# Kernel optimization log

Hardware: AMD Instinct MI355X
Metric: run time of the kernel (lower is better)

The kernel has to match this reference:

```python
import jax, jax.numpy as jnp
import numpy as np

QMIN, QMAX = -128, 127


def setup_inputs() -> dict:
    key = jax.random.key(0)
    kx, kw, kb = jax.random.split(key, 3)
    B, S, IN, OUT = 4, 2048, 4096, 4096
    x = jax.random.normal(kx, (B, S, IN), dtype=jnp.float32)
    # int8-valued weight stored as int32 for portability
    weight_int = jax.random.randint(kw, (OUT, IN), QMIN, QMAX + 1, dtype=jnp.int32)
    bias = jax.random.normal(kb, (OUT,), dtype=jnp.float32) * 0.02
    # plausible frozen qparams: x~N(0,1) -> range ~[-4,4]; weight range ~[-3,3] pre-quant
    scale_a = jnp.asarray(8.0 / 255.0, dtype=jnp.float32)
    zp_a = jnp.asarray(0, dtype=jnp.int32)
    weight_scale = jnp.asarray(6.0 / 255.0, dtype=jnp.float32)
    weight_zero_point = jnp.asarray(0, dtype=jnp.int32)
    return {
        "x": x,
        "weight_int": weight_int,
        "bias": bias,
        "scale_a": scale_a,
        "zp_a": zp_a,
        "weight_scale": weight_scale,
        "weight_zero_point": weight_zero_point,
    }


def reference(x, weight_int, bias, scale_a, zp_a, weight_scale, weight_zero_point):
    # fake-quantize activations: round(x/scale)+zp, clamp to int8 range
    zp_a_f = zp_a.astype(jnp.float32)
    x_int8 = jnp.clip(jnp.round(x / scale_a) + zp_a_f, QMIN, QMAX)
    x_cent = x_int8 - zp_a_f                                   # [B,S,IN]
    w_cent = weight_int.astype(jnp.float32) - weight_zero_point.astype(jnp.float32)  # [OUT,IN]
    y = jnp.einsum("bsi,oi->bso", x_cent, w_cent)              # dequant-space GEMM
    y = y * (scale_a * weight_scale)
    y = y + bias
    return y
```

## Files before the change

### kernel.cpp

```cpp
#include <hip/hip_runtime.h>
#include <stdint.h>

typedef int v4i  __attribute__((ext_vector_type(4)));
typedef int v16i __attribute__((ext_vector_type(16)));

__global__ void quant_x_kernel(const float* __restrict__ x,
                               int8_t* __restrict__ xq,
                               int* __restrict__ sum_x,
                               const float* __restrict__ p_scale,
                               const int* __restrict__ p_zp,
                               int K) {
    const int row = blockIdx.x;
    const int t = threadIdx.x;
    const float s = p_scale[0];
    const float zpf = (float)p_zp[0];
    const float* xr = x + (size_t)row * K;
    int8_t* qr = xq + (size_t)row * K;
    int lsum = 0;
    const int nchunk = K >> 10;
    for (int i = 0; i < nchunk; ++i) {
        const int idx = (i << 10) + (t << 2);
        const float4 v = *reinterpret_cast<const float4*>(xr + idx);
        const float f0 = fminf(fmaxf(rintf(v.x / s) + zpf, -128.f), 127.f);
        const float f1 = fminf(fmaxf(rintf(v.y / s) + zpf, -128.f), 127.f);
        const float f2 = fminf(fmaxf(rintf(v.z / s) + zpf, -128.f), 127.f);
        const float f3 = fminf(fmaxf(rintf(v.w / s) + zpf, -128.f), 127.f);
        const int i0 = (int)f0, i1 = (int)f1, i2 = (int)f2, i3 = (int)f3;
        lsum += i0 + i1 + i2 + i3;
        const unsigned pk = (unsigned)(i0 & 255) | ((unsigned)(i1 & 255) << 8) |
                            ((unsigned)(i2 & 255) << 16) | ((unsigned)(i3 & 255) << 24);
        *reinterpret_cast<unsigned*>(qr + idx) = pk;
    }
    __shared__ int wsum[4];
    #pragma unroll
    for (int off = 32; off > 0; off >>= 1) lsum += __shfl_down(lsum, off);
    if ((t & 63) == 0) wsum[t >> 6] = lsum;
    __syncthreads();
    if (t == 0) sum_x[row] = wsum[0] + wsum[1] + wsum[2] + wsum[3];
}

__global__ void quant_w_kernel(const int* __restrict__ w,
                               int8_t* __restrict__ wq,
                               int* __restrict__ sum_w,
                               int K) {
    const int row = blockIdx.x;
    const int t = threadIdx.x;
    const int* wr_ = w + (size_t)row * K;
    int8_t* qr = wq + (size_t)row * K;
    int lsum = 0;
    const int nchunk = K >> 10;
    for (int i = 0; i < nchunk; ++i) {
        const int idx = (i << 10) + (t << 2);
        const int4 v = *reinterpret_cast<const int4*>(wr_ + idx);
        lsum += v.x + v.y + v.z + v.w;
        const unsigned pk = (unsigned)(v.x & 255) | ((unsigned)(v.y & 255) << 8) |
                            ((unsigned)(v.z & 255) << 16) | ((unsigned)(v.w & 255) << 24);
        *reinterpret_cast<unsigned*>(qr + idx) = pk;
    }
    __shared__ int wsum[4];
    #pragma unroll
    for (int off = 32; off > 0; off >>= 1) lsum += __shfl_down(lsum, off);
    if ((t & 63) == 0) wsum[t >> 6] = lsum;
    __syncthreads();
    if (t == 0) sum_w[row] = wsum[0] + wsum[1] + wsum[2] + wsum[3];
}

#define BM 256
#define BN 256
#define BKB 128

__device__ __forceinline__ void gload_lds16(const void* g, void* l) {
    __builtin_amdgcn_global_load_lds(
        (const __attribute__((address_space(1))) unsigned int*)g,
        (__attribute__((address_space(3))) unsigned int*)l, 16, 0, 0);
}

#define MFMA_I8 __builtin_amdgcn_mfma_i32_32x32x32_i8

__global__ __launch_bounds__(512, 1)
void gemm_i8_kernel(const int8_t* __restrict__ xq,
                    const int8_t* __restrict__ wq,
                    const int* __restrict__ sum_x,
                    const int* __restrict__ sum_w,
                    const float* __restrict__ bias,
                    float* __restrict__ out,
                    const float* __restrict__ p_sa,
                    const int* __restrict__ p_zpa,
                    const float* __restrict__ p_sw,
                    const int* __restrict__ p_wzp,
                    int M, int N, int K) {
    __shared__ v4i ldsA[2][4][512];
    __shared__ v4i ldsB[2][4][512];

    const int tid = threadIdx.x;
    const int lane = tid & 63;
    const int wid = tid >> 6;
    const int wr = wid >> 2;
    const int wc = wid & 3;

    const int nwgy = M / BM;
    const int nwg = nwgy * (N / BN);
    const int bid = blockIdx.x;
    const int v = (bid & 7) * (nwg >> 3) + (bid >> 3);
    const int m0 = (v % nwgy) * BM;
    const int n0 = (v / nwgy) * BN;

    const int srow = wid * 32 + (lane >> 1);
    const int sj = (lane & 1) ^ ((lane >> 5) & 1);
    const int8_t* aS = xq + (size_t)(m0 + srow) * K + sj * 16;
    const int8_t* bS = wq + (size_t)(n0 + srow) * K + sj * 16;
    const int dbase = wid * 64;

    const int jp = (lane >> 5) ^ ((lane >> 4) & 1);
    const int l31 = lane & 31;
    const int aU = (wr * 128 + l31) * 2 + jp;
    const int bU = (wc * 64 + l31) * 2 + jp;

    v16i acc[4][2] = {};
    const int NT = K / BKB;

#define SLICE_STAGE(TT, S) do {                                               \
        gload_lds16(aS + (size_t)(TT) * BKB + (S) * 32,                       \
                    &ldsA[(TT) & 1][S][dbase]);                               \
        gload_lds16(bS + (size_t)(TT) * BKB + (S) * 32,                       \
                    &ldsB[(TT) & 1][S][dbase]);                               \
    } while (0)

    SLICE_STAGE(0, 0); SLICE_STAGE(0, 1); SLICE_STAGE(0, 2); SLICE_STAGE(0, 3);
    SLICE_STAGE(1, 0); SLICE_STAGE(1, 1); SLICE_STAGE(1, 2);
    asm volatile("s_waitcnt vmcnt(6)" ::: "memory");
    __builtin_amdgcn_sched_barrier(0);
    __builtin_amdgcn_s_barrier();

#define PHASE(P) do {                                                         \
        const v4i* LA = ldsA[t & 1][P];                                       \
        const v4i* LB = ldsB[t & 1][P];                                       \
        const v4i a0 = LA[aU];                                                \
        const v4i a1 = LA[aU + 64];                                           \
        const v4i a2 = LA[aU + 128];                                          \
        const v4i a3 = LA[aU + 192];                                          \
        const v4i b0 = LB[bU];                                                \
        const v4i b1 = LB[bU + 64];                                           \
        if (P == 0) { if (t <= NT - 2) SLICE_STAGE(t + 1, 3); }               \
        else        { if (t <= NT - 3) SLICE_STAGE(t + 2, P - 1); }           \
        __builtin_amdgcn_s_barrier();                                         \
        __builtin_amdgcn_s_setprio(1);                                        \
        acc[0][0] = MFMA_I8(a0, b0, acc[0][0], 0, 0, 0);                      \
        acc[0][1] = MFMA_I8(a0, b1, acc[0][1], 0, 0, 0);                      \
        acc[1][0] = MFMA_I8(a1, b0, acc[1][0], 0, 0, 0);                      \
        acc[1][1] = MFMA_I8(a1, b1, acc[1][1], 0, 0, 0);                      \
        acc[2][0] = MFMA_I8(a2, b0, acc[2][0], 0, 0, 0);                      \
        acc[2][1] = MFMA_I8(a2, b1, acc[2][1], 0, 0, 0);                      \
        acc[3][0] = MFMA_I8(a3, b0, acc[3][0], 0, 0, 0);                      \
        acc[3][1] = MFMA_I8(a3, b1, acc[3][1], 0, 0, 0);                      \
        __builtin_amdgcn_s_setprio(0);                                        \
        if (t < NT - 1) { asm volatile("s_waitcnt vmcnt(6)" ::: "memory"); }  \
        else            { asm volatile("s_waitcnt vmcnt(0)" ::: "memory"); }  \
        __builtin_amdgcn_sched_barrier(0);                                    \
        __builtin_amdgcn_s_barrier();                                         \
    } while (0)

    for (int t = 0; t < NT; ++t) {
        PHASE(0); PHASE(1); PHASE(2); PHASE(3);
    }
#undef PHASE
#undef SLICE_STAGE

    const float stot = p_sa[0] * p_sw[0];
    const int zpa = p_zpa[0];
    const int wzp = p_wzp[0];
    const int kzz = K * zpa * wzp;
    const int coll = lane & 31;
    const int rhi = (lane >> 5) * 4;

    #pragma unroll
    for (int cf = 0; cf < 2; ++cf) {
        const int cg = n0 + wc * 64 + cf * 32 + coll;
        const int sw = sum_w[cg];
        const float bb = bias[cg];
        #pragma unroll
        for (int rf = 0; rf < 4; ++rf) {
            const int rbase = m0 + wr * 128 + rf * 32 + rhi;
            #pragma unroll
            for (int r = 0; r < 16; ++r) {
                const int rowg = rbase + (r & 3) + 8 * (r >> 2);
                const int iv = acc[rf][cf][r] - wzp * sum_x[rowg] - zpa * sw + kzz;
                out[(size_t)rowg * N + cg] = (float)iv * stot + bb;
            }
        }
    }
}

extern "C" void kernel_launch(void* const* d_in, const int* in_sizes, int n_in,
                              void* d_out, int out_size, void* d_ws, size_t ws_size,
                              hipStream_t stream) {
    const float* x     = (const float*)d_in[0];
    const int*   w     = (const int*)d_in[1];
    const float* bias  = (const float*)d_in[2];
    const float* p_sa  = (const float*)d_in[3];
    const int*   p_zpa = (const int*)d_in[4];
    const float* p_sw  = (const float*)d_in[5];
    const int*   p_wzp = (const int*)d_in[6];

    const int N = in_sizes[2];
    const int K = in_sizes[1] / N;
    const int M = in_sizes[0] / K;

    int8_t* xq = (int8_t*)d_ws;
    int8_t* wq = xq + (size_t)M * K;
    int* sum_x = (int*)(wq + (size_t)N * K);
    int* sum_w = sum_x + M;

    quant_x_kernel<<<M, 256, 0, stream>>>(x, xq, sum_x, p_sa, p_zpa, K);
    quant_w_kernel<<<N, 256, 0, stream>>>(w, wq, sum_w, K);

    const int nwg = (M / BM) * (N / BN);
    gemm_i8_kernel<<<nwg, 512, 0, stream>>>(xq, wq, sum_x, sum_w, bias,
                                            (float*)d_out, p_sa, p_zpa, p_sw, p_wzp,
                                            M, N, K);
}
```

Before: 263.2 us.

## Load A fragments directly to registers and stage only B through LDS

The int8 GEMM no longer stages the activation tile through shared memory. Each wave loads its A fragments straight from global memory into registers, double-buffered across K steps. Only the weight tile goes through LDS, now with K-step 64 and an XOR swizzle. This cuts LDS traffic and footprint and halves the per-iteration barrier count, at the cost of more global traffic for A (redundant across the four column waves) and a full vmcnt(0) wait every tile, which gives shallower prefetch.

```diff
diff --git a/kernel.cpp b/kernel.cpp
--- a/kernel.cpp
+++ b/kernel.cpp
@@ -67,7 +67,7 @@
 
 #define BM 256
 #define BN 256
-#define BKB 128
+#define BKB 64
 
 __device__ __forceinline__ void gload_lds16(const void* g, void* l) {
     __builtin_amdgcn_global_load_lds(
@@ -89,8 +89,7 @@
                     const float* __restrict__ p_sw,
                     const int* __restrict__ p_wzp,
                     int M, int N, int K) {
-    __shared__ v4i ldsA[2][4][512];
-    __shared__ v4i ldsB[2][4][512];
+    __shared__ v4i ldsB[2][1024];
 
     const int tid = threadIdx.x;
     const int lane = tid & 63;
@@ -105,66 +104,83 @@
     const int m0 = (v % nwgy) * BM;
     const int n0 = (v / nwgy) * BN;
 
-    const int srow = wid * 32 + (lane >> 1);
-    const int sj = (lane & 1) ^ ((lane >> 5) & 1);
-    const int8_t* aS = xq + (size_t)(m0 + srow) * K + sj * 16;
-    const int8_t* bS = wq + (size_t)(n0 + srow) * K + sj * 16;
+    const int srow = tid >> 2;
+    const int schunk = (tid & 3) ^ (((srow >> 1) ^ (srow >> 3)) & 3);
+    const int8_t* bS = wq + (size_t)(n0 + srow) * K + schunk * 16;
+    const size_t half = (size_t)128 * K;
     const int dbase = wid * 64;
 
-    const int jp = (lane >> 5) ^ ((lane >> 4) & 1);
-    const int l31 = lane & 31;
-    const int aU = (wr * 128 + l31) * 2 + jp;
-    const int bU = (wc * 64 + l31) * 2 + jp;
+    const int sel = ((lane >> 1) ^ (lane >> 3)) & 3;
+    const int hi = lane >> 5;
+    const int bbase = (wc * 64 + (lane & 31)) * 4;
+    const int c00 = hi ^ sel;
+    const int c01 = (2 + hi) ^ sel;
+
+    const int8_t* aP = xq + (size_t)(m0 + wr * 128 + (lane & 31)) * K + ((lane >> 5) << 4);
+    const size_t arf = (size_t)32 * K;
 
     v16i acc[4][2] = {};
+    v4i afA[8], afB[8];
+
     const int NT = K / BKB;
 
-#define SLICE_STAGE(TT, S) do {                                               \
-        gload_lds16(aS + (size_t)(TT) * BKB + (S) * 32,                       \
-                    &ldsA[(TT) & 1][S][dbase]);                               \
-        gload_lds16(bS + (size_t)(TT) * BKB + (S) * 32,                       \
-                    &ldsB[(TT) & 1][S][dbase]);                               \
-    } while (0)
-
-    SLICE_STAGE(0, 0); SLICE_STAGE(0, 1); SLICE_STAGE(0, 2); SLICE_STAGE(0, 3);
-    SLICE_STAGE(1, 0); SLICE_STAGE(1, 1); SLICE_STAGE(1, 2);
-    asm volatile("s_waitcnt vmcnt(6)" ::: "memory");
+    gload_lds16(bS,        &ldsB[0][dbase]);
+    gload_lds16(bS + half, &ldsB[0][dbase + 512]);
+    #pragma unroll
+    for (int rf = 0; rf < 4; ++rf) {
+        afA[rf * 2 + 0] = *reinterpret_cast<const v4i*>(aP + rf * arf);
+        afA[rf * 2 + 1] = *reinterpret_cast<const v4i*>(aP + rf * arf + 32);
+    }
+    asm volatile("s_waitcnt vmcnt(0)" ::: "memory");
     __builtin_amdgcn_sched_barrier(0);
     __builtin_amdgcn_s_barrier();
 
-#define PHASE(P) do {                                                         \
-        const v4i* LA = ldsA[t & 1][P];                                       \
-        const v4i* LB = ldsB[t & 1][P];                                       \
-        const v4i a0 = LA[aU];                                                \
-        const v4i a1 = LA[aU + 64];                                           \
-        const v4i a2 = LA[aU + 128];                                          \
-        const v4i a3 = LA[aU + 192];                                          \
-        const v4i b0 = LB[bU];                                                \
-        const v4i b1 = LB[bU + 64];                                           \
-        if (P == 0) { if (t <= NT - 2) SLICE_STAGE(t + 1, 3); }               \
-        else        { if (t <= NT - 3) SLICE_STAGE(t + 2, P - 1); }           \
-        __builtin_amdgcn_s_barrier();                                         \
+#define TILE(ACUR, ANXT, T_) do {                                             \
+        const int t_ = (T_);                                                  \
+        const v4i* LB = ldsB[t_ & 1];                                         \
+        const v4i b00 = LB[bbase + c00];                                      \
+        const v4i b01 = LB[bbase + c01];                                      \
+        const v4i b10 = LB[bbase + 128 + c00];                                \
+        const v4i b11 = LB[bbase + 128 + c01];                                \
+        if (t_ + 1 < NT) {                                                    \
+            const int8_t* pb = bS + (size_t)(t_ + 1) * BKB;                   \
+            gload_lds16(pb,        &ldsB[(t_ + 1) & 1][dbase]);               \
+            gload_lds16(pb + half, &ldsB[(t_ + 1) & 1][dbase + 512]);         \
+            const int8_t* pa = aP + (size_t)(t_ + 1) * BKB;                   \
+            _Pragma("unroll")                                                 \
+            for (int rf = 0; rf < 4; ++rf) {                                  \
+                ANXT[rf * 2 + 0] = *reinterpret_cast<const v4i*>(pa + rf * arf);      \
+                ANXT[rf * 2 + 1] = *reinterpret_cast<const v4i*>(pa + rf * arf + 32); \
+            }                                                                 \
+        }                                                                     \
         __builtin_amdgcn_s_setprio(1);                                        \
-        acc[0][0] = MFMA_I8(a0, b0, acc[0][0], 0, 0, 0);                      \
-        acc[0][1] = MFMA_I8(a0, b1, acc[0][1], 0, 0, 0);                      \
-        acc[1][0] = MFMA_I8(a1, b0, acc[1][0], 0, 0, 0);                      \
-        acc[1][1] = MFMA_I8(a1, b1, acc[1][1], 0, 0, 0);                      \
-        acc[2][0] = MFMA_I8(a2, b0, acc[2][0], 0, 0, 0);                      \
-        acc[2][1] = MFMA_I8(a2, b1, acc[2][1], 0, 0, 0);                      \
-        acc[3][0] = MFMA_I8(a3, b0, acc[3][0], 0, 0, 0);                      \
-        acc[3][1] = MFMA_I8(a3, b1, acc[3][1], 0, 0, 0);                      \
+        acc[0][0] = MFMA_I8(ACUR[0], b00, acc[0][0], 0, 0, 0);                \
+        acc[0][1] = MFMA_I8(ACUR[0], b10, acc[0][1], 0, 0, 0);                \
+        acc[1][0] = MFMA_I8(ACUR[2], b00, acc[1][0], 0, 0, 0);                \
+        acc[1][1] = MFMA_I8(ACUR[2], b10, acc[1][1], 0, 0, 0);                \
+        acc[2][0] = MFMA_I8(ACUR[4], b00, acc[2][0], 0, 0, 0);                \
+        acc[2][1] = MFMA_I8(ACUR[4], b10, acc[2][1], 0, 0, 0);                \
+        acc[3][0] = MFMA_I8(ACUR[6], b00, acc[3][0], 0, 0, 0);                \
+        acc[3][1] = MFMA_I8(ACUR[6], b10, acc[3][1], 0, 0, 0);                \
+        acc[0][0] = MFMA_I8(ACUR[1], b01, acc[0][0], 0, 0, 0);                \
+        acc[0][1] = MFMA_I8(ACUR[1], b11, acc[0][1], 0, 0, 0);                \
+        acc[1][0] = MFMA_I8(ACUR[3], b01, acc[1][0], 0, 0, 0);                \
+        acc[1][1] = MFMA_I8(ACUR[3], b11, acc[1][1], 0, 0, 0);                \
+        acc[2][0] = MFMA_I8(ACUR[5], b01, acc[2][0], 0, 0, 0);                \
+        acc[2][1] = MFMA_I8(ACUR[5], b11, acc[2][1], 0, 0, 0);                \
+        acc[3][0] = MFMA_I8(ACUR[7], b01, acc[3][0], 0, 0, 0);                \
+        acc[3][1] = MFMA_I8(ACUR[7], b11, acc[3][1], 0, 0, 0);                \
         __builtin_amdgcn_s_setprio(0);                                        \
-        if (t < NT - 1) { asm volatile("s_waitcnt vmcnt(6)" ::: "memory"); }  \
-        else            { asm volatile("s_waitcnt vmcnt(0)" ::: "memory"); }  \
+        asm volatile("s_waitcnt vmcnt(0)" ::: "memory");                      \
         __builtin_amdgcn_sched_barrier(0);                                    \
         __builtin_amdgcn_s_barrier();                                         \
     } while (0)
 
-    for (int t = 0; t < NT; ++t) {
-        PHASE(0); PHASE(1); PHASE(2); PHASE(3);
-    }
-#undef PHASE
-#undef SLICE_STAGE
+    for (int tt = 0; tt < NT; tt += 2) {
+        TILE(afA, afB, tt);
+        TILE(afB, afA, tt + 1);
+    }
+#undef TILE
 
     const float stot = p_sa[0] * p_sw[0];
     const int zpa = p_zpa[0];
```

Result: slower. 394.8 us (+50.0%).
